# Kernel optimization log

Measured on AMD Instinct MI355X. Metric: run time of the kernel, lower is better.

Reference implementation:

```python
import jax, jax.numpy as jnp
import numpy as np

B, L, D, H = 2, 2048, 1024, 16
HD = D // H
EPS = 1e-6

def _rms(x, w):
    return x * jax.lax.rsqrt(jnp.mean(x * x, axis=-1, keepdims=True) + EPS) * w

def _lin(x, w, b=None):
    y = x @ w.T
    return y if b is None else y + b

def setup_inputs() -> dict:
    key = jax.random.key(0)
    ks = jax.random.split(key, 16)
    def w(i, shape, s=0.02):
        return jax.random.normal(ks[i], shape, dtype=jnp.float32) * s
    return dict(
        z=jax.random.normal(ks[0], (B, L, D), dtype=jnp.float32),
        connection=jax.random.normal(ks[1], (B, L, D), dtype=jnp.float32),
        w_z=jnp.ones(D, jnp.float32), w_c=jnp.ones(D, jnp.float32), w_mlp=jnp.ones(D, jnp.float32),
        f_w1=w(2, (2 * D, D)), f_b1=jnp.zeros(2 * D, jnp.float32),
        f_w2=w(3, (D, 2 * D)), f_b2=jnp.zeros(D, jnp.float32),
        g_w1=w(4, (D, 2 * D)), g_b1=jnp.zeros(D, jnp.float32),
        g_w2=w(5, (D, D)), g_b2=jnp.zeros(D, jnp.float32),
        dt=jnp.float32(0.1),
        q_w=w(6, (D, 2 * D)), k_w=w(7, (D, 2 * D)), v_w=w(8, (D, D)), o_w=w(9, (D, D)),
        temp=jnp.float32(1.0),
        cu_w1=w(10, (2 * D, 3 * D)), cu_b1=jnp.zeros(2 * D, jnp.float32),
        cu_w2=w(11, (D, 2 * D)), cu_b2=jnp.zeros(D, jnp.float32),
        m_w1=w(12, (4 * D, D)), m_b1=jnp.zeros(4 * D, jnp.float32),
        m_w2=w(13, (D, 4 * D)), m_b2=jnp.zeros(D, jnp.float32),
    )

def reference(z, connection, w_z, w_c, w_mlp,
              f_w1, f_b1, f_w2, f_b2, g_w1, g_b1, g_w2, g_b2, dt,
              q_w, k_w, v_w, o_w, temp,
              cu_w1, cu_b1, cu_w2, cu_b2,
              m_w1, m_b1, m_w2, m_b2):
    z_before = z
    zn = _rms(z, w_z)
    cn = _rms(connection, w_c)

    # covariant vector field: dz = dt * (F(zn) + gamma(cat(cn, F(zn))))
    dz_local = _lin(jax.nn.silu(_lin(zn, f_w1, f_b1)), f_w2, f_b2)
    corr = _lin(jnp.tanh(_lin(jnp.concatenate([cn, dz_local], -1), g_w1, g_b1)), g_w2, g_b2)
    dz = dt * (dz_local + corr)

    # covariant sigmoid attention
    zc = jnp.concatenate([zn, cn], -1)                       # [B,L,2D]
    Q = _lin(zc, q_w).reshape(B, L, H, HD).transpose(0, 2, 1, 3)  # bhld
    K = _lin(zc, k_w).reshape(B, L, H, HD).transpose(0, 2, 1, 3)
    V = _lin(zn, v_w).reshape(B, L, H, HD).transpose(0, 2, 1, 3)
    scores = jnp.einsum('bhld,bhmd->bhlm', Q, K) * (HD ** -0.5) * temp
    rel = jax.nn.sigmoid(scores)
    rel_sum = jnp.clip(jnp.sum(rel, -1, keepdims=True), 1.0, None)
    attn = jnp.einsum('bhlm,bhmd->bhld', rel, V) / rel_sum
    ctx = _lin(attn.transpose(0, 2, 1, 3).reshape(B, L, D), o_w)

    z1 = z + dz + ctx

    # connection update
    delta = _lin(jax.nn.silu(_lin(jnp.concatenate([connection, z1, dz], -1), cu_w1, cu_b1)), cu_w2, cu_b2)
    conn_new = connection + delta

    # MLP block
    z2 = z1 + _lin(jax.nn.silu(_lin(_rms(z1, w_mlp), m_w1, m_b1)), m_w2, m_b2)
    return (z2, conn_new, z_before)
```

## Files before the change

kernel.cpp:

```cpp
#include <hip/hip_runtime.h>


typedef unsigned short u16;
typedef __attribute__((ext_vector_type(8))) short short8;
typedef __attribute__((ext_vector_type(8))) unsigned short us8;
typedef __attribute__((ext_vector_type(4))) float f32x4;
typedef __attribute__((ext_vector_type(4))) unsigned short us4;
typedef __attribute__((ext_vector_type(2))) unsigned int u32x2;

__device__ __forceinline__ float b2f(u16 u) {
    union { unsigned u; float f; } c; c.u = ((unsigned)u) << 16; return c.f;
}
__device__ __forceinline__ u16 f2b(float f) {
    union { float f; unsigned u; } c; c.f = f;
    unsigned x = c.u;
    unsigned r = (x + 0x7fffu + ((x >> 16) & 1u)) >> 16;
    return (u16)r;
}
__device__ __forceinline__ float fast_rcp(float x) {
    return __builtin_amdgcn_rcpf(x);
}
__device__ __forceinline__ unsigned cvt_pk_bf16(float a, float b) {
    unsigned r;
    asm("v_cvt_pk_bf16_f32 %0, %1, %2" : "=v"(r) : "v"(a), "v"(b));
    return r;
}

__device__ __forceinline__ void async_copy16(const u16* g, u16* l) {
    __builtin_amdgcn_global_load_lds(
        (const __attribute__((address_space(1))) unsigned int*)(g),
        (__attribute__((address_space(3))) unsigned int*)(l), 16, 0, 0);
}

__global__ __launch_bounds__(256) void cvt_k(const float* __restrict__ s,
                                             u16* __restrict__ d, int n) {
    int i = (blockIdx.x * 256 + threadIdx.x) * 4;
    if (i >= n) return;
    f32x4 v = *(const f32x4*)(s + i);
    us4 o;
#pragma unroll
    for (int k = 0; k < 4; k++) o[k] = f2b(v[k]);
    *(us4*)(d + i) = o;
}

__global__ __launch_bounds__(256) void rmsf_k(const float* __restrict__ x,
                                              const float* __restrict__ w,
                                              u16* __restrict__ y,
                                              float* __restrict__ cp,
                                              u16* __restrict__ cb, int D) {
    int n = blockIdx.x;
    const float* xr = x + (size_t)n * D;
    int i0 = threadIdx.x << 2;
    f32x4 v = *(const f32x4*)(xr + i0);
    if (cp) *(f32x4*)(cp + (size_t)n * D + i0) = v;
    if (cb) {
        us4 o2;
#pragma unroll
        for (int k = 0; k < 4; k++) o2[k] = f2b(v[k]);
        *(us4*)(cb + (size_t)n * D + i0) = o2;
    }
    float s = v[0] * v[0] + v[1] * v[1] + v[2] * v[2] + v[3] * v[3];
#pragma unroll
    for (int m = 32; m >= 1; m >>= 1) s += __shfl_xor(s, m, 64);
    __shared__ float red[4];
    if ((threadIdx.x & 63) == 0) red[threadIdx.x >> 6] = s;
    __syncthreads();
    float tot = red[0] + red[1] + red[2] + red[3];
    float scale = rsqrtf(tot / (float)D + 1e-6f);
    f32x4 wv = *(const f32x4*)(w + i0);
    us4 o;
#pragma unroll
    for (int k = 0; k < 4; k++) o[k] = f2b(v[k] * scale * wv[k]);
    *(us4*)(y + (size_t)n * D + i0) = o;
}

__global__ __launch_bounds__(256) void rmsb_k(const u16* __restrict__ x,
                                              const float* __restrict__ w,
                                              u16* __restrict__ y, int D) {
    int n = blockIdx.x;
    const u16* xr = x + (size_t)n * D;
    int i0 = threadIdx.x << 2;
    us4 xv = *(const us4*)(xr + i0);
    float v[4]; float s = 0.f;
#pragma unroll
    for (int k = 0; k < 4; k++) { v[k] = b2f(xv[k]); s += v[k] * v[k]; }
#pragma unroll
    for (int m = 32; m >= 1; m >>= 1) s += __shfl_xor(s, m, 64);
    __shared__ float red[4];
    if ((threadIdx.x & 63) == 0) red[threadIdx.x >> 6] = s;
    __syncthreads();
    float tot = red[0] + red[1] + red[2] + red[3];
    float scale = rsqrtf(tot / (float)D + 1e-6f);
    f32x4 wv = *(const f32x4*)(w + i0);
    us4 o;
#pragma unroll
    for (int k = 0; k < 4; k++) o[k] = f2b(v[k] * scale * wv[k]);
    *(us4*)(y + (size_t)n * D + i0) = o;
}

template <int BN, int NSEG>
__global__ __launch_bounds__(256) void gemm_t(const u16* __restrict__ A0,
                                              const u16* __restrict__ A1,
                                              const u16* __restrict__ A2,
                                              const u16* __restrict__ W,
                                              const float* __restrict__ bias,
                                              u16* __restrict__ C,
                                              int K, int O, int act, int mode) {
    constexpr int NJ = BN / 32;
    constexpr int WN = BN / 2;
    __shared__ u16 Asm[2][128 * 64];
    __shared__ u16 Bsm[2][BN * 64];

    const int tid = threadIdx.x;
    const int wid = tid >> 6, lane = tid & 63;
    const int l15 = lane & 15, quad = lane >> 4;
    const int lsw = l15 & 7;

    const int nwg = gridDim.x * gridDim.y;
    int id = blockIdx.y * gridDim.x + blockIdx.x;
    id = (id & 7) * (nwg >> 3) + (id >> 3);
    const int bx = id % gridDim.x, by = id / gridDim.x;

    const int row0 = by * 128, col0 = bx * BN;
    const int wm = (wid >> 1) << 6, wn = (wid & 1) * WN;

    const int rb = tid >> 3;
    const int gg = ((tid & 7) ^ (rb & 7)) << 3;
    const int sA = (NSEG == 1) ? K : 1024;
    const size_t aoff = (size_t)(row0 + rb) * sA + gg;
    const size_t boff = (size_t)(col0 + rb) * K + gg;
    const int ldsb = wid << 9;

    f32x4 acc[4][NJ];
#pragma unroll
    for (int i = 0; i < 4; i++)
#pragma unroll
        for (int j = 0; j < NJ; j++) acc[i][j] = (f32x4){0.f, 0.f, 0.f, 0.f};

    auto stage = [&](int buf, int kof) {
        const u16* Ab; int kcol;
        if constexpr (NSEG == 1) { Ab = A0; kcol = kof; }
        else {
            int seg = kof >> 10;
            Ab = (seg == 0) ? A0 : ((NSEG == 3 && seg == 2) ? A2 : A1);
            kcol = kof & 1023;
        }
        const u16* as = Ab + aoff + kcol;
        const u16* bs = W + boff + kof;
#pragma unroll
        for (int i = 0; i < 4; i++)
            async_copy16(as + (size_t)(32 * i) * sA, &Asm[buf][(i << 11) + ldsb]);
#pragma unroll
        for (int i = 0; i < BN / 32; i++)
            async_copy16(bs + (size_t)(32 * i) * K, &Bsm[buf][(i << 11) + ldsb]);
    };

    const int nk = K >> 6;
    stage(0, 0);
    __syncthreads();
    for (int kk = 0; kk < nk; kk++) {
        int cur = kk & 1;
        if (kk + 1 < nk) stage(1 - cur, (kk + 1) << 6);
        const u16* Ab = Asm[cur];
        const u16* Bb = Bsm[cur];
#pragma unroll
        for (int h = 0; h < 2; h++) {
            const int gq = (((h << 2) + quad) ^ lsw) << 3;
            short8 af[4], bf[NJ];
#pragma unroll
            for (int i = 0; i < 4; i++)
                af[i] = *(const short8*)&Ab[(wm + i * 16 + l15) * 64 + gq];
#pragma unroll
            for (int j = 0; j < NJ; j++)
                bf[j] = *(const short8*)&Bb[(wn + j * 16 + l15) * 64 + gq];
#pragma unroll
            for (int i = 0; i < 4; i++)
#pragma unroll
                for (int j = 0; j < NJ; j++)
                    acc[i][j] = __builtin_amdgcn_mfma_f32_16x16x32_bf16(af[i], bf[j], acc[i][j], 0, 0, 0);
        }
        __syncthreads();
    }

    if (mode == 0) {
#pragma unroll
        for (int j = 0; j < NJ; j++) {
            int col = col0 + wn + j * 16 + l15;
            float bb = bias ? bias[col] : 0.f;
#pragma unroll
            for (int i = 0; i < 4; i++) {
                int rowb = row0 + wm + i * 16 + (quad << 2);
#pragma unroll
                for (int g = 0; g < 4; g++) {
                    float v = acc[i][j][g] + bb;
                    if (act == 1) {
                        v = v * fast_rcp(1.f + __expf(-v));
                    } else if (act == 2) {
                        float t = __expf(v * 2.f);
                        v = 1.f - 2.f * fast_rcp(1.f + t);
                    }
                    C[(size_t)(rowb + g) * O + col] = f2b(v);
                }
            }
        }
    } else {
#pragma unroll
        for (int j = 0; j < NJ; j++) {
            int col = col0 + wn + j * 16 + l15;
            int h = col >> 6, d = col & 63;
#pragma unroll
            for (int i = 0; i < 4; i++) {
                int rowb = row0 + wm + i * 16 + (quad << 2);
                int bb_ = rowb >> 11;
                int tok = rowb & 2047;
                u32x2 pk2;
                pk2[0] = cvt_pk_bf16(acc[i][j][0], acc[i][j][1]);
                pk2[1] = cvt_pk_bf16(acc[i][j][2], acc[i][j][3]);
                *(u32x2*)&C[(size_t)(((bb_ << 4) + h) * 64 + d) * 2048 + tok] = pk2;
            }
        }
    }
}

__global__ __launch_bounds__(256) void attn_k(const u16* __restrict__ QK,
                                              const u16* __restrict__ VT,
                                              const float* __restrict__ temp_p,
                                              u16* __restrict__ Oa) {
    const int L = 2048, D = 1024, SQ = 2048;
    __shared__ u16 Ks[2][64 * 64];
    __shared__ u16 Vs[2][64 * 64];
    __shared__ u16 plds[4][16 * 72];

    const int tid = threadIdx.x;
    const int w = tid >> 6, lane = tid & 63;
    const int l15 = lane & 15, quad = lane >> 4;
    int id = blockIdx.x;
    id = (id & 7) * 64 + (id >> 3);
    const int bh = id >> 4;
    const int qb0 = (id & 15) << 7;
    const int b = bh >> 4, h = bh & 15;
    const float nsc2 = -0.125f * temp_p[0] * 1.44269504f;

    short8 aq[2][2];
#pragma unroll
    for (int qt = 0; qt < 2; qt++) {
        size_t row = (size_t)(b * L + qb0 + w * 32 + qt * 16 + l15) * SQ + h * 64;
#pragma unroll
        for (int hf = 0; hf < 2; hf++)
            aq[qt][hf] = *(const short8*)(QK + row + hf * 32 + quad * 8);
    }

    const u16* Kbase = QK + 1024 + (size_t)(b * L) * SQ + h * 64;
    const u16* VTb   = VT + (size_t)bh * 64 * L;

    const int i0 = tid, i1 = tid + 256;
    const int r0 = i0 >> 3, g0 = (i0 & 7) ^ (r0 & 7);
    const int r1 = i1 >> 3, g1 = (i1 & 7) ^ (r1 & 7);
    const u16* kS0 = Kbase + (size_t)r0 * SQ + g0 * 8;
    const u16* kS1 = Kbase + (size_t)r1 * SQ + g1 * 8;
    const u16* vS0 = VTb + (size_t)r0 * L + g0 * 8;
    const u16* vS1 = VTb + (size_t)r1 * L + g1 * 8;

    auto stage = [&](int buf, int mc) {
        async_copy16(kS0 + (size_t)mc * SQ, &Ks[buf][w << 9]);
        async_copy16(kS1 + (size_t)mc * SQ, &Ks[buf][2048 + (w << 9)]);
        async_copy16(vS0 + mc, &Vs[buf][w << 9]);
        async_copy16(vS1 + mc, &Vs[buf][2048 + (w << 9)]);
    };

    f32x4 acc[2][4];
#pragma unroll
    for (int i = 0; i < 2; i++)
#pragma unroll
        for (int j = 0; j < 4; j++) acc[i][j] = (f32x4){0.f, 0.f, 0.f, 0.f};
    float rs[2] = {0.f, 0.f};
    u16* P = plds[w];
    const int lsw = l15 & 7;

    stage(0, 0);
    __syncthreads();
    for (int it = 0; it < 32; it++) {
        int cur = it & 1;
        if (it < 31) stage(1 - cur, (it + 1) << 6);
        const u16* Kt = Ks[cur];
        const u16* Vt = Vs[cur];
#pragma unroll
        for (int qt = 0; qt < 2; qt++) {
#pragma unroll
            for (int ks = 0; ks < 4; ks++) {
                f32x4 s = (f32x4){0.f, 0.f, 0.f, 0.f};
#pragma unroll
                for (int hf = 0; hf < 2; hf++) {
                    int slot = ((ks * 16 + l15) * 8 + ((hf * 4 + quad) ^ lsw)) * 8;
                    short8 bk = *(const short8*)&Kt[slot];
                    s = __builtin_amdgcn_mfma_f32_16x16x32_bf16(bk, aq[qt][hf], s, 0, 0, 0);
                }
                float p0 = fast_rcp(1.f + __builtin_amdgcn_exp2f(s[0] * nsc2));
                float p1 = fast_rcp(1.f + __builtin_amdgcn_exp2f(s[1] * nsc2));
                float p2 = fast_rcp(1.f + __builtin_amdgcn_exp2f(s[2] * nsc2));
                float p3 = fast_rcp(1.f + __builtin_amdgcn_exp2f(s[3] * nsc2));
                rs[qt] += (p0 + p1) + (p2 + p3);
                u32x2 pk2;
                pk2[0] = cvt_pk_bf16(p0, p1);
                pk2[1] = cvt_pk_bf16(p2, p3);
                *(u32x2*)&P[l15 * 72 + ks * 16 + (quad << 2)] = pk2;
            }
#pragma unroll
            for (int kh = 0; kh < 2; kh++) {
                short8 ap = *(const short8*)&P[l15 * 72 + kh * 32 + quad * 8];
#pragma unroll
                for (int dt = 0; dt < 4; dt++) {
                    int slot = ((dt * 16 + l15) * 8 + ((kh * 4 + quad) ^ lsw)) * 8;
                    short8 bv = *(const short8*)&Vt[slot];
                    acc[qt][dt] = __builtin_amdgcn_mfma_f32_16x16x32_bf16(ap, bv, acc[qt][dt], 0, 0, 0);
                }
            }
        }
        __syncthreads();
    }

#pragma unroll
    for (int qt = 0; qt < 2; qt++) {
        rs[qt] += __shfl_xor(rs[qt], 16, 64);
        rs[qt] += __shfl_xor(rs[qt], 32, 64);
    }

#pragma unroll
    for (int qt = 0; qt < 2; qt++) {
        u16* orow = Oa + (size_t)(b * L + qb0 + w * 32 + qt * 16) * D + h * 64;
#pragma unroll
        for (int g = 0; g < 4; g++) {
            int row = quad * 4 + g;
            float denom = __shfl(rs[qt], row, 64);
            float rd = fast_rcp(fmaxf(denom, 1.0f));
#pragma unroll
            for (int dt = 0; dt < 4; dt++)
                orow[(size_t)row * D + dt * 16 + l15] = f2b(acc[qt][dt][g] * rd);
        }
    }
}

__global__ void dz_k(u16* __restrict__ d, const u16* __restrict__ a,
                     const u16* __restrict__ b, const float* __restrict__ dtp, int n) {
    int i = (blockIdx.x * 256 + threadIdx.x) * 8;
    if (i >= n) return;
    float dt = dtp[0];
    us8 va = *(const us8*)(a + i), vb = *(const us8*)(b + i);
    us8 o;
#pragma unroll
    for (int k = 0; k < 8; k++) o[k] = f2b(dt * (b2f(va[k]) + b2f(vb[k])));
    *(us8*)(d + i) = o;
}

__global__ void z1_k(u16* __restrict__ d, const float* __restrict__ z,
                     const u16* __restrict__ dz, const u16* __restrict__ ctx, int n) {
    int i = (blockIdx.x * 256 + threadIdx.x) * 8;
    if (i >= n) return;
    f32x4 z0 = *(const f32x4*)(z + i), z4 = *(const f32x4*)(z + i + 4);
    us8 vd = *(const us8*)(dz + i), vc = *(const us8*)(ctx + i);
    us8 o;
#pragma unroll
    for (int k = 0; k < 4; k++) {
        o[k]     = f2b(z0[k] + b2f(vd[k])     + b2f(vc[k]));
        o[k + 4] = f2b(z4[k] + b2f(vd[k + 4]) + b2f(vc[k + 4]));
    }
    *(us8*)(d + i) = o;
}

__global__ void connew_k(float* __restrict__ d, const float* __restrict__ conn,
                         const u16* __restrict__ delta, int n) {
    int i = (blockIdx.x * 256 + threadIdx.x) * 8;
    if (i >= n) return;
    f32x4 c0 = *(const f32x4*)(conn + i), c4 = *(const f32x4*)(conn + i + 4);
    us8 vd = *(const us8*)(delta + i);
    f32x4 o0, o4;
#pragma unroll
    for (int k = 0; k < 4; k++) {
        o0[k] = c0[k] + b2f(vd[k]);
        o4[k] = c4[k] + b2f(vd[k + 4]);
    }
    *(f32x4*)(d + i) = o0;
    *(f32x4*)(d + i + 4) = o4;
}

__global__ void z2_k(float* __restrict__ d, const u16* __restrict__ z1,
                     const u16* __restrict__ mf, int n) {
    int i = (blockIdx.x * 256 + threadIdx.x) * 8;
    if (i >= n) return;
    us8 va = *(const us8*)(z1 + i), vb = *(const us8*)(mf + i);
    f32x4 o0, o4;
#pragma unroll
    for (int k = 0; k < 4; k++) {
        o0[k] = b2f(va[k]) + b2f(vb[k]);
        o4[k] = b2f(va[k + 4]) + b2f(vb[k + 4]);
    }
    *(f32x4*)(d + i) = o0;
    *(f32x4*)(d + i + 4) = o4;
}

extern "C" void kernel_launch(void* const* d_in, const int* in_sizes, int n_in,
                              void* d_out, int out_size, void* d_ws, size_t ws_size,
                              hipStream_t stream) {
    const int B = 2, L = 2048, D = 1024, H = 16, N = B * L;
    const float* z      = (const float*)d_in[0];
    const float* conn   = (const float*)d_in[1];
    const float* w_z    = (const float*)d_in[2];
    const float* w_c    = (const float*)d_in[3];
    const float* w_mlp  = (const float*)d_in[4];
    const float* f_w1   = (const float*)d_in[5];
    const float* f_b1   = (const float*)d_in[6];
    const float* f_w2   = (const float*)d_in[7];
    const float* f_b2   = (const float*)d_in[8];
    const float* g_w1   = (const float*)d_in[9];
    const float* g_b1   = (const float*)d_in[10];
    const float* g_w2   = (const float*)d_in[11];
    const float* g_b2   = (const float*)d_in[12];
    const float* dt_p   = (const float*)d_in[13];
    const float* q_w    = (const float*)d_in[14];
    const float* k_w    = (const float*)d_in[15];
    const float* v_w    = (const float*)d_in[16];
    const float* o_w    = (const float*)d_in[17];
    const float* temp_p = (const float*)d_in[18];
    const float* cu_w1  = (const float*)d_in[19];
    const float* cu_b1  = (const float*)d_in[20];
    const float* cu_w2  = (const float*)d_in[21];
    const float* cu_b2  = (const float*)d_in[22];
    const float* m_w1   = (const float*)d_in[23];
    const float* m_b1   = (const float*)d_in[24];
    const float* m_w2   = (const float*)d_in[25];
    const float* m_b2   = (const float*)d_in[26];

    float* out = (float*)d_out;
    u16* ws  = (u16*)d_ws;
    const size_t U = (size_t)N * D;

    u16* zn    = ws + 0 * U;
    u16* cn    = ws + 1 * U;
    u16* h1    = ws + 2 * U;
    u16* dzl   = ws + 4 * U;
    u16* gh    = ws + 5 * U;
    u16* corr  = ws + 6 * U;
    u16* dz    = ws + 7 * U;
    u16* connb = ws + 8 * U;
    u16* QK    = ws + 2 * U;
    u16* VT    = ws + 4 * U;
    u16* attnb = ws + 1 * U;
    u16* ctx   = ws + 4 * U;
    u16* z1    = ws + 5 * U;
    u16* cu_h  = ws + 2 * U;
    u16* delta = ws + 1 * U;
    u16* z1n   = ws + 0 * U;
    u16* mh    = ws + 1 * U;
    u16* mf    = ws + 6 * U;

    u16* wb = ws + 9 * U;
    u16* bf_w1  = wb + 0;
    u16* bf_w2  = wb + 2 * 1024 * 1024;
    u16* bg_w1  = wb + 4 * 1024 * 1024;
    u16* bg_w2  = wb + 6 * 1024 * 1024;
    u16* bqk_w  = wb + 7 * 1024 * 1024;
    u16* bv_w   = wb + 11 * 1024 * 1024;
    u16* bo_w   = wb + 12 * 1024 * 1024;
    u16* bcu_w1 = wb + 13 * 1024 * 1024;
    u16* bcu_w2 = wb + 19 * 1024 * 1024;
    u16* bm_w1  = wb + 21 * 1024 * 1024;
    u16* bm_w2  = wb + 25 * 1024 * 1024;

    auto cvt = [&](const float* s, u16* d, int n) {
        cvt_k<<<n / 1024, 256, 0, stream>>>(s, d, n);
    };
    cvt(f_w1, bf_w1, 2 * D * D);   cvt(f_w2, bf_w2, 2 * D * D);
    cvt(g_w1, bg_w1, 2 * D * D);   cvt(g_w2, bg_w2, D * D);
    cvt(q_w, bqk_w, 2 * D * D);    cvt(k_w, bqk_w + 2 * D * D, 2 * D * D);
    cvt(v_w, bv_w, D * D);         cvt(o_w, bo_w, D * D);
    cvt(cu_w1, bcu_w1, 6 * D * D); cvt(cu_w2, bcu_w2, 2 * D * D);
    cvt(m_w1, bm_w1, 4 * D * D);   cvt(m_w2, bm_w2, 4 * D * D);

    const int EW8 = (N * D / 8 + 255) / 256;
    auto gemm = [&](const u16* A, const u16* W, const float* bias, u16* C,
                    int K, int O, int act, int mode = 0) {
        if (O == 1024) {
            dim3 grid(16, 32);
            gemm_t<64, 1><<<grid, 256, 0, stream>>>(A, nullptr, nullptr, W, bias, C, K, O, act, mode);
        } else {
            dim3 grid(O / 128, 32);
            gemm_t<128, 1><<<grid, 256, 0, stream>>>(A, nullptr, nullptr, W, bias, C, K, O, act, mode);
        }
    };

    rmsf_k<<<N, 256, 0, stream>>>(z, w_z, zn, out + 2 * U, nullptr, D);
    rmsf_k<<<N, 256, 0, stream>>>(conn, w_c, cn, nullptr, connb, D);

    gemm(zn, bf_w1, f_b1, h1, D, 2 * D, 1);
    gemm(h1, bf_w2, f_b2, dzl, 2 * D, D, 0);
    gemm_t<64, 2><<<dim3(16, 32), 256, 0, stream>>>(
        cn, dzl, nullptr, bg_w1, g_b1, gh, 2 * D, D, 2, 0);
    gemm(gh, bg_w2, g_b2, corr, D, D, 0);
    dz_k<<<EW8, 256, 0, stream>>>(dz, dzl, corr, dt_p, N * D);

    gemm_t<128, 2><<<dim3(16, 32), 256, 0, stream>>>(
        zn, cn, nullptr, bqk_w, nullptr, QK, 2 * D, 2 * D, 0, 0);
    gemm(zn, bv_w, nullptr, VT, D, D, 0, 1);
    attn_k<<<B * H * L / 128, 256, 0, stream>>>(QK, VT, temp_p, attnb);
    gemm(attnb, bo_w, nullptr, ctx, D, D, 0);

    z1_k<<<EW8, 256, 0, stream>>>(z1, z, dz, ctx, N * D);

    gemm_t<128, 3><<<dim3(16, 32), 256, 0, stream>>>(
        connb, z1, dz, bcu_w1, cu_b1, cu_h, 3 * D, 2 * D, 1, 0);
    gemm(cu_h, bcu_w2, cu_b2, delta, 2 * D, D, 0);
    connew_k<<<EW8, 256, 0, stream>>>(out + U, conn, delta, N * D);

    rmsb_k<<<N, 256, 0, stream>>>(z1, w_mlp, z1n, D);
    gemm(z1n, bm_w1, m_b1, mh, D, 4 * D, 1);
    gemm(mh, bm_w2, m_b2, mf, 4 * D, D, 0);
    z2_k<<<EW8, 256, 0, stream>>>(out, z1, mf, N * D);
}
```

Baseline: 729.9 us.

## Fuse elementwise residual ops into GEMM epilogues and shrink GEMM tiles

Four standalone elementwise kernels (dz, z1, conn_new, z2) are removed. Their work now runs in new GEMM epilogue modes that read the extra operands and write bf16 or fp32 output directly. The GEMM template also gains a BM parameter, and tiles shrink to 128x64 or 64x64, which roughly doubles to quadruples the block count to improve CU occupancy and load balance. The trade-off is less data reuse per block and more branching in the epilogue.

```diff
diff --git a/kernel.cpp b/kernel.cpp
--- a/kernel.cpp
+++ b/kernel.cpp
@@ -98,17 +98,21 @@
     *(us4*)(y + (size_t)n * D + i0) = o;
 }
 
-template <int BN, int NSEG>
+template <int BM, int BN, int NSEG>
 __global__ __launch_bounds__(256) void gemm_t(const u16* __restrict__ A0,
                                               const u16* __restrict__ A1,
                                               const u16* __restrict__ A2,
                                               const u16* __restrict__ W,
                                               const float* __restrict__ bias,
                                               u16* __restrict__ C,
+                                              const u16* __restrict__ Eb,
+                                              const float* __restrict__ Ef,
+                                              const float* __restrict__ sc,
+                                              float* __restrict__ Cf,
                                               int K, int O, int act, int mode) {
-    constexpr int NJ = BN / 32;
-    constexpr int WN = BN / 2;
-    __shared__ u16 Asm[2][128 * 64];
+    constexpr int WM = BM / 2, WN = BN / 2;
+    constexpr int NI = WM / 16, NJ = WN / 16;
+    __shared__ u16 Asm[2][BM * 64];
     __shared__ u16 Bsm[2][BN * 64];
 
     const int tid = threadIdx.x;
@@ -121,8 +125,8 @@
     id = (id & 7) * (nwg >> 3) + (id >> 3);
     const int bx = id % gridDim.x, by = id / gridDim.x;
 
-    const int row0 = by * 128, col0 = bx * BN;
-    const int wm = (wid >> 1) << 6, wn = (wid & 1) * WN;
+    const int row0 = by * BM, col0 = bx * BN;
+    const int wm = (wid >> 1) * WM, wn = (wid & 1) * WN;
 
     const int rb = tid >> 3;
     const int gg = ((tid & 7) ^ (rb & 7)) << 3;
@@ -131,9 +135,9 @@
     const size_t boff = (size_t)(col0 + rb) * K + gg;
     const int ldsb = wid << 9;
 
-    f32x4 acc[4][NJ];
-#pragma unroll
-    for (int i = 0; i < 4; i++)
+    f32x4 acc[NI][NJ];
+#pragma unroll
+    for (int i = 0; i < NI; i++)
 #pragma unroll
         for (int j = 0; j < NJ; j++) acc[i][j] = (f32x4){0.f, 0.f, 0.f, 0.f};
 
@@ -148,7 +152,7 @@
         const u16* as = Ab + aoff + kcol;
         const u16* bs = W + boff + kof;
 #pragma unroll
-        for (int i = 0; i < 4; i++)
+        for (int i = 0; i < BM / 32; i++)
             async_copy16(as + (size_t)(32 * i) * sA, &Asm[buf][(i << 11) + ldsb]);
 #pragma unroll
         for (int i = 0; i < BN / 32; i++)
@@ -166,15 +170,15 @@
 #pragma unroll
         for (int h = 0; h < 2; h++) {
             const int gq = (((h << 2) + quad) ^ lsw) << 3;
-            short8 af[4], bf[NJ];
-#pragma unroll
-            for (int i = 0; i < 4; i++)
+            short8 af[NI], bf[NJ];
+#pragma unroll
+            for (int i = 0; i < NI; i++)
                 af[i] = *(const short8*)&Ab[(wm + i * 16 + l15) * 64 + gq];
 #pragma unroll
             for (int j = 0; j < NJ; j++)
                 bf[j] = *(const short8*)&Bb[(wn + j * 16 + l15) * 64 + gq];
 #pragma unroll
-            for (int i = 0; i < 4; i++)
+            for (int i = 0; i < NI; i++)
 #pragma unroll
                 for (int j = 0; j < NJ; j++)
                     acc[i][j] = __builtin_amdgcn_mfma_f32_16x16x32_bf16(af[i], bf[j], acc[i][j], 0, 0, 0);
@@ -182,13 +186,30 @@
         __syncthreads();
     }
 
-    if (mode == 0) {
+    if (mode == 1) {
+#pragma unroll
+        for (int j = 0; j < NJ; j++) {
+            int col = col0 + wn + j * 16 + l15;
+            int h = col >> 6, d = col & 63;
+#pragma unroll
+            for (int i = 0; i < NI; i++) {
+                int rowb = row0 + wm + i * 16 + (quad << 2);
+                int bb_ = rowb >> 11;
+                int tok = rowb & 2047;
+                u32x2 pk2;
+                pk2[0] = cvt_pk_bf16(acc[i][j][0], acc[i][j][1]);
+                pk2[1] = cvt_pk_bf16(acc[i][j][2], acc[i][j][3]);
+                *(u32x2*)&C[(size_t)(((bb_ << 4) + h) * 64 + d) * 2048 + tok] = pk2;
+            }
+        }
+    } else {
+        float dtv = (mode == 2) ? sc[0] : 0.f;
 #pragma unroll
         for (int j = 0; j < NJ; j++) {
             int col = col0 + wn + j * 16 + l15;
             float bb = bias ? bias[col] : 0.f;
 #pragma unroll
-            for (int i = 0; i < 4; i++) {
+            for (int i = 0; i < NI; i++) {
                 int rowb = row0 + wm + i * 16 + (quad << 2);
 #pragma unroll
                 for (int g = 0; g < 4; g++) {
@@ -199,24 +220,13 @@
                         float t = __expf(v * 2.f);
                         v = 1.f - 2.f * fast_rcp(1.f + t);
                     }
-                    C[(size_t)(rowb + g) * O + col] = f2b(v);
+                    size_t idx = (size_t)(rowb + g) * O + col;
+                    if (mode == 0)      C[idx] = f2b(v);
+                    else if (mode == 2) C[idx] = f2b(dtv * (b2f(Eb[idx]) + v));
+                    else if (mode == 3) C[idx] = f2b(Ef[idx] + b2f(Eb[idx]) + v);
+                    else if (mode == 4) Cf[idx] = Ef[idx] + v;
+                    else                Cf[idx] = b2f(Eb[idx]) + v;
                 }
-            }
-        }
-    } else {
-#pragma unroll
-        for (int j = 0; j < NJ; j++) {
-            int col = col0 + wn + j * 16 + l15;
-            int h = col >> 6, d = col & 63;
-#pragma unroll
-            for (int i = 0; i < 4; i++) {
-                int rowb = row0 + wm + i * 16 + (quad << 2);
-                int bb_ = rowb >> 11;
-                int tok = rowb & 2047;
-                u32x2 pk2;
-                pk2[0] = cvt_pk_bf16(acc[i][j][0], acc[i][j][1]);
-                pk2[1] = cvt_pk_bf16(acc[i][j][2], acc[i][j][3]);
-                *(u32x2*)&C[(size_t)(((bb_ << 4) + h) * 64 + d) * 2048 + tok] = pk2;
             }
         }
     }
@@ -338,64 +348,6 @@
                 orow[(size_t)row * D + dt * 16 + l15] = f2b(acc[qt][dt][g] * rd);
         }
     }
-}
-
-__global__ void dz_k(u16* __restrict__ d, const u16* __restrict__ a,
-                     const u16* __restrict__ b, const float* __restrict__ dtp, int n) {
-    int i = (blockIdx.x * 256 + threadIdx.x) * 8;
-    if (i >= n) return;
-    float dt = dtp[0];
-    us8 va = *(const us8*)(a + i), vb = *(const us8*)(b + i);
-    us8 o;
-#pragma unroll
-    for (int k = 0; k < 8; k++) o[k] = f2b(dt * (b2f(va[k]) + b2f(vb[k])));
-    *(us8*)(d + i) = o;
-}
-
-__global__ void z1_k(u16* __restrict__ d, const float* __restrict__ z,
-                     const u16* __restrict__ dz, const u16* __restrict__ ctx, int n) {
-    int i = (blockIdx.x * 256 + threadIdx.x) * 8;
-    if (i >= n) return;
-    f32x4 z0 = *(const f32x4*)(z + i), z4 = *(const f32x4*)(z + i + 4);
-    us8 vd = *(const us8*)(dz + i), vc = *(const us8*)(ctx + i);
-    us8 o;
-#pragma unroll
-    for (int k = 0; k < 4; k++) {
-        o[k]     = f2b(z0[k] + b2f(vd[k])     + b2f(vc[k]));
-        o[k + 4] = f2b(z4[k] + b2f(vd[k + 4]) + b2f(vc[k + 4]));
-    }
-    *(us8*)(d + i) = o;
-}
-
-__global__ void connew_k(float* __restrict__ d, const float* __restrict__ conn,
-                         const u16* __restrict__ delta, int n) {
-    int i = (blockIdx.x * 256 + threadIdx.x) * 8;
-    if (i >= n) return;
-    f32x4 c0 = *(const f32x4*)(conn + i), c4 = *(const f32x4*)(conn + i + 4);
-    us8 vd = *(const us8*)(delta + i);
-    f32x4 o0, o4;
-#pragma unroll
-    for (int k = 0; k < 4; k++) {
-        o0[k] = c0[k] + b2f(vd[k]);
-        o4[k] = c4[k] + b2f(vd[k + 4]);
-    }
-    *(f32x4*)(d + i) = o0;
-    *(f32x4*)(d + i + 4) = o4;
-}
-
-__global__ void z2_k(float* __restrict__ d, const u16* __restrict__ z1,
-                     const u16* __restrict__ mf, int n) {
-    int i = (blockIdx.x * 256 + threadIdx.x) * 8;
-    if (i >= n) return;
-    us8 va = *(const us8*)(z1 + i), vb = *(const us8*)(mf + i);
-    f32x4 o0, o4;
-#pragma unroll
-    for (int k = 0; k < 4; k++) {
-        o0[k] = b2f(va[k]) + b2f(vb[k]);
-        o4[k] = b2f(va[k + 4]) + b2f(vb[k + 4]);
-    }
-    *(f32x4*)(d + i) = o0;
-    *(f32x4*)(d + i + 4) = o4;
 }
 
 extern "C" void kernel_launch(void* const* d_in, const int* in_sizes, int n_in,
@@ -439,19 +391,15 @@
     u16* h1    = ws + 2 * U;
     u16* dzl   = ws + 4 * U;
     u16* gh    = ws + 5 * U;
-    u16* corr  = ws + 6 * U;
-    u16* dz    = ws + 7 * U;
-    u16* connb = ws + 8 * U;
+    u16* dz    = ws + 6 * U;
+    u16* connb = ws + 7 * U;
     u16* QK    = ws + 2 * U;
     u16* VT    = ws + 4 * U;
     u16* attnb = ws + 1 * U;
-    u16* ctx   = ws + 4 * U;
     u16* z1    = ws + 5 * U;
     u16* cu_h  = ws + 2 * U;
-    u16* delta = ws + 1 * U;
     u16* z1n   = ws + 0 * U;
     u16* mh    = ws + 1 * U;
-    u16* mf    = ws + 6 * U;
 
     u16* wb = ws + 9 * U;
     u16* bf_w1  = wb + 0;
@@ -476,43 +424,36 @@
     cvt(cu_w1, bcu_w1, 6 * D * D); cvt(cu_w2, bcu_w2, 2 * D * D);
     cvt(m_w1, bm_w1, 4 * D * D);   cvt(m_w2, bm_w2, 4 * D * D);
 
-    const int EW8 = (N * D / 8 + 255) / 256;
-    auto gemm = [&](const u16* A, const u16* W, const float* bias, u16* C,
-                    int K, int O, int act, int mode = 0) {
-        if (O == 1024) {
-            dim3 grid(16, 32);
-            gemm_t<64, 1><<<grid, 256, 0, stream>>>(A, nullptr, nullptr, W, bias, C, K, O, act, mode);
-        } else {
-            dim3 grid(O / 128, 32);
-            gemm_t<128, 1><<<grid, 256, 0, stream>>>(A, nullptr, nullptr, W, bias, C, K, O, act, mode);
-        }
-    };
-
     rmsf_k<<<N, 256, 0, stream>>>(z, w_z, zn, out + 2 * U, nullptr, D);
     rmsf_k<<<N, 256, 0, stream>>>(conn, w_c, cn, nullptr, connb, D);
 
-    gemm(zn, bf_w1, f_b1, h1, D, 2 * D, 1);
-    gemm(h1, bf_w2, f_b2, dzl, 2 * D, D, 0);
-    gemm_t<64, 2><<<dim3(16, 32), 256, 0, stream>>>(
-        cn, dzl, nullptr, bg_w1, g_b1, gh, 2 * D, D, 2, 0);
-    gemm(gh, bg_w2, g_b2, corr, D, D, 0);
-    dz_k<<<EW8, 256, 0, stream>>>(dz, dzl, corr, dt_p, N * D);
-
-    gemm_t<128, 2><<<dim3(16, 32), 256, 0, stream>>>(
-        zn, cn, nullptr, bqk_w, nullptr, QK, 2 * D, 2 * D, 0, 0);
-    gemm(zn, bv_w, nullptr, VT, D, D, 0, 1);
+    const u16* nu = nullptr;
+    gemm_t<128, 64, 1><<<dim3(32, 32), 256, 0, stream>>>(
+        zn, nu, nu, bf_w1, f_b1, h1, nu, nullptr, nullptr, nullptr, D, 2 * D, 1, 0);
+    gemm_t<64, 64, 1><<<dim3(16, 64), 256, 0, stream>>>(
+        h1, nu, nu, bf_w2, f_b2, dzl, nu, nullptr, nullptr, nullptr, 2 * D, D, 0, 0);
+    gemm_t<64, 64, 2><<<dim3(16, 64), 256, 0, stream>>>(
+        cn, dzl, nu, bg_w1, g_b1, gh, nu, nullptr, nullptr, nullptr, 2 * D, D, 2, 0);
+    gemm_t<64, 64, 1><<<dim3(16, 64), 256, 0, stream>>>(
+        gh, nu, nu, bg_w2, g_b2, dz, dzl, nullptr, dt_p, nullptr, D, D, 0, 2);
+
+    gemm_t<128, 64, 2><<<dim3(32, 32), 256, 0, stream>>>(
+        zn, cn, nu, bqk_w, nullptr, QK, nu, nullptr, nullptr, nullptr, 2 * D, 2 * D, 0, 0);
+    gemm_t<64, 64, 1><<<dim3(16, 64), 256, 0, stream>>>(
+        zn, nu, nu, bv_w, nullptr, VT, nu, nullptr, nullptr, nullptr, D, D, 0, 1);
     attn_k<<<B * H * L / 128, 256, 0, stream>>>(QK, VT, temp_p, attnb);
-    gemm(attnb, bo_w, nullptr, ctx, D, D, 0);
-
-    z1_k<<<EW8, 256, 0, stream>>>(z1, z, dz, ctx, N * D);
-
-    gemm_t<128, 3><<<dim3(16, 32), 256, 0, stream>>>(
-        connb, z1, dz, bcu_w1, cu_b1, cu_h, 3 * D, 2 * D, 1, 0);
-    gemm(cu_h, bcu_w2, cu_b2, delta, 2 * D, D, 0);
-    connew_k<<<EW8, 256, 0, stream>>>(out + U, conn, delta, N * D);
+    gemm_t<64, 64, 1><<<dim3(16, 64), 256, 0, stream>>>(
+        attnb, nu, nu, bo_w, nullptr, z1, dz, z, nullptr, nullptr, D, D, 0, 3);
+
+    gemm_t<128, 64, 3><<<dim3(32, 32), 256, 0, stream>>>(
+        connb, z1, dz, bcu_w1, cu_b1, cu_h, nu, nullptr, nullptr, nullptr, 3 * D, 2 * D, 1, 0);
+    gemm_t<64, 64, 1><<<dim3(16, 64), 256, 0, stream>>>(
+        cu_h, nu, nu, bcu_w2, cu_b2, nu == nullptr ? (u16*)nullptr : (u16*)nullptr,
+        nu, conn, nullptr, out + U, 2 * D, D, 0, 4);
 
     rmsb_k<<<N, 256, 0, stream>>>(z1, w_mlp, z1n, D);
-    gemm(z1n, bm_w1, m_b1, mh, D, 4 * D, 1);
-    gemm(mh, bm_w2, m_b2, mf, 4 * D, D, 0);
-    z2_k<<<EW8, 256, 0, stream>>>(out, z1, mf, N * D);
-}
+    gemm_t<128, 64, 1><<<dim3(64, 32), 256, 0, stream>>>(
+        z1n, nu, nu, bm_w1, m_b1, mh, nu, nullptr, nullptr, nullptr, D, 4 * D, 1, 0);
+    gemm_t<64, 64, 1><<<dim3(16, 64), 256, 0, stream>>>(
+        mh, nu, nu, bm_w2, m_b2, (u16*)nullptr, z1, nullptr, nullptr, out, 4 * D, D, 0, 5);
+}
```

New measurement: 764.8 us. 4.8% more time.
